# Kernel tuning notes

Hardware: AMD Instinct MI355X
Metric: run time of the kernel (lower is better)

The kernel has to match this reference:

```python
import jax, jax.numpy as jnp
import numpy as np

H = 128          # hidden
L = 4            # num PNA layers
NG = 32          # graphs in the batch
OUT = 12
N_NODES = 30000
N_EDGES = 480000
IN_NODE = 64
IN_EDGE = 16
EPS_BN = 1e-5
EPS_STD = 1e-5
# deg histogram torch.tensor([1,2,3,4,5,6]): cnt_i nodes have degree i
_cnt = np.arange(1.0, 7.0)
AVG_LOG = float((np.log(np.arange(6) + 1.0) * _cnt).sum() / _cnt.sum())


def _lin(k, fan_in, fan_out):
    return jax.random.normal(k, (fan_in, fan_out), jnp.float32) * 0.05


def setup_inputs() -> dict:
    key = jax.random.key(0)
    ks = jax.random.split(key, 16)
    d = {}
    d["x"] = jax.random.normal(ks[0], (N_NODES, IN_NODE), jnp.float32)
    d["edge_attr"] = jax.random.normal(ks[1], (N_EDGES, IN_EDGE), jnp.float32)
    d["edge_index"] = jax.random.randint(ks[2], (2, N_EDGES), 0, N_NODES)
    d["batch"] = jnp.sort(jax.random.randint(ks[3], (N_NODES,), 0, NG))
    d["node_emb_W"] = _lin(ks[4], IN_NODE, H)
    d["node_emb_b"] = jnp.zeros((H,), jnp.float32)
    d["edge_emb_W"] = _lin(ks[5], IN_EDGE, H)
    d["edge_emb_b"] = jnp.zeros((H,), jnp.float32)
    kl = jax.random.split(ks[6], 4 * L)
    d["edge_enc_W"] = jnp.stack([_lin(kl[i], H, H) for i in range(L)])
    d["edge_enc_b"] = jnp.zeros((L, H), jnp.float32)
    d["pre_W"] = jnp.stack([_lin(kl[L + i], 3 * H, H) for i in range(L)])
    d["pre_b"] = jnp.zeros((L, H), jnp.float32)
    d["post_W"] = jnp.stack([_lin(kl[2 * L + i], 13 * H, H) for i in range(L)])
    d["post_b"] = jnp.zeros((L, H), jnp.float32)
    d["lin_W"] = jnp.stack([_lin(kl[3 * L + i], H, H) for i in range(L)])
    d["lin_b"] = jnp.zeros((L, H), jnp.float32)
    d["bn_gamma"] = jnp.ones((L, H), jnp.float32)
    d["bn_beta"] = jnp.zeros((L, H), jnp.float32)
    d["head1_W"] = _lin(ks[7], H, H // 2)
    d["head1_b"] = jnp.zeros((H // 2,), jnp.float32)
    d["head2_W"] = _lin(ks[8], H // 2, OUT)
    d["head2_b"] = jnp.zeros((OUT,), jnp.float32)
    return d


def _pna_layer(x, e, src, dst, eW, eb, pW, pb, oW, ob, lW, lb):
    n = x.shape[0]
    ee = e @ eW + eb                                      # edge encoder [E, H]
    h = jnp.concatenate([x[dst], x[src], ee], axis=-1)    # (x_i, x_j, e) [E, 3H]
    m = h @ pW + pb                                       # pre-nn messages [E, H]
    ones = jnp.ones((m.shape[0],), m.dtype)
    deg = jax.ops.segment_sum(ones, dst, num_segments=n)  # in-degree [N]
    degc = jnp.maximum(deg, 1.0)[:, None]
    has = (deg > 0.0)[:, None]
    mean = jax.ops.segment_sum(m, dst, num_segments=n) / degc
    mn = jnp.where(has, jax.ops.segment_min(m, dst, num_segments=n), 0.0)
    mx = jnp.where(has, jax.ops.segment_max(m, dst, num_segments=n), 0.0)
    mean_sq = jax.ops.segment_sum(m * m, dst, num_segments=n) / degc
    std = jnp.sqrt(jax.nn.relu(mean_sq - mean * mean) + EPS_STD)
    agg = jnp.concatenate([mean, mn, mx, std], axis=-1)   # aggregators [N, 4H]
    amp = jnp.log(degc + 1.0) / AVG_LOG                   # amplification scale
    out = jnp.concatenate([agg, agg * amp, agg / amp], axis=-1)  # id/amp/atten [N, 12H]
    out = jnp.concatenate([x, out], axis=-1) @ oW + ob    # post-nn [N, H]
    return out @ lW + lb                                  # final lin


def reference(x, edge_index, batch, edge_attr, node_emb_W, node_emb_b,
              edge_emb_W, edge_emb_b, edge_enc_W, edge_enc_b, pre_W, pre_b,
              post_W, post_b, lin_W, lin_b, bn_gamma, bn_beta,
              head1_W, head1_b, head2_W, head2_b):
    src, dst = edge_index[0], edge_index[1]
    h = x @ node_emb_W + node_emb_b
    e = edge_attr @ edge_emb_W + edge_emb_b
    for l in range(L):
        h = _pna_layer(h, e, src, dst, edge_enc_W[l], edge_enc_b[l],
                       pre_W[l], pre_b[l], post_W[l], post_b[l],
                       lin_W[l], lin_b[l])
        mu = h.mean(axis=0)
        var = h.var(axis=0)  # biased, as BatchNorm training-mode normalization
        h = (h - mu) / jnp.sqrt(var + EPS_BN) * bn_gamma[l] + bn_beta[l]
        h = jax.nn.relu(h)   # dropout == identity (eval mode reference)
    g = jax.ops.segment_sum(h, batch, num_segments=NG)   # global_add_pool [NG, H]
    z = jax.nn.relu(g @ head1_W + head1_b)
    return z @ head2_W + head2_b
```

## Files before the change

kernel.cpp:

```cpp
#include <hip/hip_runtime.h>
#include <hip/hip_bf16.h>
#include <math.h>

#define NN 30000
#define NE 480000
#define NLAYER 4
#define NGR 32
#define NOUT 12
#define EPS_BN 1e-5f
#define EPS_STD 1e-5f
#define AVG_LOG 1.3821454785305053f
#define MB_GRID 235

typedef unsigned short ushort_t;
typedef __bf16 bf16x8 __attribute__((ext_vector_type(8)));
typedef float floatx4 __attribute__((ext_vector_type(4)));

__device__ __forceinline__ float bfu(ushort_t u){
  union { unsigned int ui; float f; } c; c.ui = ((unsigned int)u) << 16; return c.f;
}
__device__ __forceinline__ ushort_t f2bf(float f){
  union { float f; unsigned int u; } c; c.f = f;
  unsigned int lsb = (c.u >> 16) & 1u;
  c.u += 0x7FFFu + lsb;
  return (ushort_t)(c.u >> 16);
}

__device__ __forceinline__ int plausible(unsigned int bits32){
  unsigned int e = (bits32 >> 23) & 0xFF;
  if(e == 0xFF) return 0;
  if(bits32 == 0 || bits32 == 0x80000000u) return 1;
  return (e >= 93 && e <= 140) ? 1 : 0;
}

__global__ void k_detect(const ushort_t* __restrict__ xr, int* __restrict__ flag){
  __shared__ int cnt[2];
  if(threadIdx.x < 2) cnt[threadIdx.x] = 0;
  __syncthreads();
  const unsigned int* xf = (const unsigned int*)xr;
  int gf = 0, gb = 0;
  for(int i = threadIdx.x; i < 1024; i += 256){
    gf += plausible(xf[i]);
    gb += plausible(((unsigned int)xr[i]) << 16);
  }
  atomicAdd(&cnt[0], gf);
  atomicAdd(&cnt[1], gb);
  __syncthreads();
  if(threadIdx.x == 0) *flag = (cnt[1] >= cnt[0]) ? 1 : 0;
}

#define NJOBS 18
struct CvtJob { const void* s; float* d; int n; };
struct CvtArgs { CvtJob j[NJOBS]; const int* flag; };

__global__ void k_cvt(CvtArgs a){
  int ji = blockIdx.y;
  const int isbf = *a.flag;
  float* d = a.j[ji].d;
  int n = a.j[ji].n;
  if(isbf){
    const ushort_t* s = (const ushort_t*)a.j[ji].s;
    for(int i = blockIdx.x*256 + threadIdx.x; i < n; i += gridDim.x*256) d[i] = bfu(s[i]);
  } else {
    const float* s = (const float*)a.j[ji].s;
    for(int i = blockIdx.x*256 + threadIdx.x; i < n; i += gridDim.x*256) d[i] = s[i];
  }
}

__global__ void k_xbf(const void* __restrict__ x, ushort_t* __restrict__ d,
                      const int* __restrict__ flag){
  int i = blockIdx.x*256 + threadIdx.x;
  if(i >= NN*64) return;
  if(*flag) d[i] = ((const ushort_t*)x)[i];
  else      d[i] = f2bf(((const float*)x)[i]);
}

#define NTR 9
struct TrJob { const float* s; ushort_t* d; int K, N; };
struct TrArgs { TrJob j[NTR]; };

__global__ void k_tr(TrArgs a){
  TrJob j = a.j[blockIdx.y];
  int nk = j.K >> 6, nn = j.N >> 6;
  int tile = blockIdx.x;
  if(tile >= nk*nn) return;
  int tk = tile % nk, tn = tile / nk;
  int k0 = tk*64, n0 = tn*64;
  __shared__ float t[64][65];
  int w = threadIdx.x >> 6, c = threadIdx.x & 63;
  #pragma unroll
  for(int i=0;i<16;i+=1){
    int r = i*4 + w;
    t[r][c] = j.s[(size_t)(k0+r)*j.N + n0 + c];
  }
  __syncthreads();
  #pragma unroll
  for(int i=0;i<16;i+=1){
    int r = i*4 + w;
    j.d[(size_t)(n0+r)*j.K + k0 + c] = f2bf(t[c][r]);
  }
}

#define NFOLD 16
struct FoldJob { const float* s1; const float* s2; ushort_t* d; int Kd; };
struct FoldArgs { FoldJob j[NFOLD]; };

__global__ void k_fold(FoldArgs a){
  FoldJob j = a.j[blockIdx.y];
  const int n0 = blockIdx.x*16;
  __shared__ float s2s[128][16];
  int tid = threadIdx.x;
  for(int idx = tid; idx < 128*16; idx += 256){
    int t = idx >> 4, jj = idx & 15;
    s2s[t][jj] = j.s2[t*128 + n0 + jj];
  }
  __syncthreads();
  for(int k = tid; k < j.Kd; k += 256){
    float part[16];
    #pragma unroll
    for(int p=0;p<16;p++) part[p] = 0.f;
    for(int t0=0; t0<128; t0+=32){
      float rr[32];
      #pragma unroll
      for(int tt=0;tt<32;tt++) rr[tt] = j.s1[(size_t)k*128 + t0 + tt];
      #pragma unroll
      for(int p=0;p<16;p++){
        float acc = 0.f;
        #pragma unroll
        for(int tt=0;tt<32;tt++) acc += rr[tt]*s2s[t0+tt][p];
        part[p] += acc;
      }
    }
    #pragma unroll
    for(int p=0;p<16;p++)
      j.d[(size_t)(n0+p)*j.Kd + k] = f2bf(part[p]);
  }
}

__global__ void k_foldb(const float* __restrict__ postB, const float* __restrict__ linW,
                        const float* __restrict__ linB, float* __restrict__ biasY){
  int l = blockIdx.x, c = threadIdx.x;
  float a = linB[l*128+c];
  const float* L = linW + (size_t)l*128*128;
  const float* pb = postB + l*128;
  for(int t=0;t<128;t++) a += pb[t]*L[t*128+c];
  biasY[l*128+c] = a;
}

__global__ void k_deg(const int* __restrict__ dst, int* __restrict__ deg){
  int i = blockIdx.x*256 + threadIdx.x;
  if(i < NE){
    unsigned d = (unsigned)dst[i];
    if(d < NN) atomicAdd(&deg[d], 1);
  }
}

__global__ void k_scan1(const int* __restrict__ deg, int* __restrict__ rp,
                        int* __restrict__ bsum){
  __shared__ int wsum[16];
  int tid = threadIdx.x, lane = tid & 63, wid = tid >> 6;
  int i = blockIdx.x*1024 + tid;
  int v = (i < NN) ? deg[i] : 0;
  int incl = v;
  #pragma unroll
  for(int off=1; off<64; off<<=1){
    int t = __shfl_up(incl, off, 64);
    if(lane >= off) incl += t;
  }
  if(lane==63) wsum[wid] = incl;
  __syncthreads();
  int woff = 0;
  for(int w=0; w<wid; w++) woff += wsum[w];
  if(i < NN) rp[i+1] = incl + woff;
  if(tid == 0){
    int t = 0;
    for(int w=0; w<16; w++) t += wsum[w];
    bsum[blockIdx.x] = t;
  }
}

__global__ void k_scan2(const int* __restrict__ bsum, int* __restrict__ boff,
                        int* __restrict__ rp, int nb){
  if(threadIdx.x == 0){
    int run = 0;
    for(int b=0;b<nb;b++){ boff[b] = run; run += bsum[b]; }
    rp[0] = 0;
  }
}

__global__ void k_scan3(int* __restrict__ rp, const int* __restrict__ boff){
  int i = blockIdx.x*1024 + threadIdx.x;
  if(i < NN) rp[i+1] += boff[blockIdx.x];
}

__global__ void k_scatter(const int* __restrict__ dst,
                          const int* __restrict__ rp, int* __restrict__ fill,
                          int* __restrict__ eix_csr){
  int i = blockIdx.x*256 + threadIdx.x;
  if(i >= NE) return;
  unsigned d = (unsigned)dst[i];
  if(d >= NN) return;
  int pos = rp[d] + atomicAdd(&fill[d], 1);
  eix_csr[pos] = i;
}

__launch_bounds__(64)
__global__ void k_srt(const int* __restrict__ rp, int* __restrict__ eix){
  __shared__ int buf[64][129];
  int t = threadIdx.x;
  int n = blockIdx.x*64 + t;
  if(n >= NN) return;
  int s0 = rp[n], e0 = rp[n+1], d = e0 - s0;
  if(d <= 1) return;
  if(d <= 128){
    int* b = buf[t];
    for(int i=0;i<d;i++) b[i] = eix[s0+i];
    for(int i=1;i<d;i++){
      int k = b[i], j = i-1;
      while(j >= 0 && b[j] > k){ b[j+1] = b[j]; j--; }
      b[j+1] = k;
    }
    for(int i=0;i<d;i++) eix[s0+i] = b[i];
  } else {
    for(int i=s0+1;i<e0;i++){
      int k = eix[i], j = i-1;
      while(j >= s0 && eix[j] > k){ eix[j+1] = eix[j]; j--; }
      eix[j+1] = k;
    }
  }
}

__global__ void k_gather_ea(const int* __restrict__ eix, const int* __restrict__ esrc,
                            const void* __restrict__ ea,
                            ushort_t* __restrict__ out, int* __restrict__ src_csr,
                            const int* __restrict__ flag){
  int j = blockIdx.x*128 + threadIdx.x;
  if(j >= NE) return;
  int i = eix[j];
  src_csr[j] = esrc[i];
  uint4* d = (uint4*)(out + (size_t)j*16);
  if(*flag){
    const uint4* s = (const uint4*)((const ushort_t*)ea + (size_t)i*16);
    d[0] = s[0]; d[1] = s[1];
  } else {
    const float* s = (const float*)ea + (size_t)i*16;
    union { ushort_t us[16]; uint4 u4[2]; } pk;
    #pragma unroll
    for(int k=0;k<16;k++) pk.us[k] = f2bf(s[k]);
    d[0] = pk.u4[0]; d[1] = pk.u4[1];
  }
}

__global__ void k_prep_K(const float* __restrict__ embW, const float* __restrict__ embB,
                         const float* __restrict__ encW, const float* __restrict__ encB,
                         const float* __restrict__ preW, const float* __restrict__ preB,
                         float* __restrict__ Kf){
  int bx = blockIdx.x;
  int l = bx / 17, r = bx % 17;
  int c = threadIdx.x;
  const float* eW = encW + (size_t)l*128*128;
  const float* P3 = preW + (size_t)l*384*128 + 256*128;
  __shared__ float trow[128];
  float a;
  if(r < 16){
    a = 0.f;
    const float* w = embW + r*128;
    for(int k=0;k<128;k++) a += w[k]*eW[k*128+c];
  } else {
    a = encB[l*128+c];
    for(int k=0;k<128;k++) a += embB[k]*eW[k*128+c];
  }
  trow[c] = a;
  __syncthreads();
  float o = (r==16) ? preB[l*128+c] : 0.f;
  for(int k=0;k<128;k++) o += trow[k]*P3[k*128+c];
  Kf[(size_t)l*17*128 + r*128 + c] = o;
}

template<int EPI, int OUTBF>
__launch_bounds__(256)
__global__ void k_mm(const ushort_t* __restrict__ A, const ushort_t* __restrict__ BT,
                     void* __restrict__ C, void* __restrict__ C2,
                     int M, int K, int ldc, const float* __restrict__ bias){
  __shared__ __align__(16) ushort_t Als[128][88];
  __shared__ __align__(16) ushort_t Bls[128][88];
  const int tid = threadIdx.x;
  const int m0 = blockIdx.x*128, n0 = blockIdx.y*128;
  const int w = tid >> 6, lane = tid & 63;
  const int wm = (w & 1)*64, wn = (w >> 1)*64;
  const int quad = lane >> 4, l15 = lane & 15;
  floatx4 acc[4][4] = {};

  for(int k0=0; k0<K; k0+=64){
    #pragma unroll
    for(int i=0;i<4;i++){
      int c = tid + 256*i;
      int row = c >> 3, kc = (c & 7)*8;
      uint4 va = make_uint4(0u,0u,0u,0u);
      int gr = m0 + row;
      if(gr < M) va = *(const uint4*)(A + (size_t)gr*K + k0 + kc);
      *(uint4*)(&Als[row][kc]) = va;
      uint4 vb = *(const uint4*)(BT + (size_t)(n0+row)*K + k0 + kc);
      *(uint4*)(&Bls[row][kc]) = vb;
    }
    __syncthreads();
    #pragma unroll
    for(int ks=0; ks<64; ks+=32){
      bf16x8 a[4], b[4];
      #pragma unroll
      for(int i=0;i<4;i++) a[i] = *(const bf16x8*)(&Als[wm+16*i+l15][ks+quad*8]);
      #pragma unroll
      for(int j=0;j<4;j++) b[j] = *(const bf16x8*)(&Bls[wn+16*j+l15][ks+quad*8]);
      #pragma unroll
      for(int i=0;i<4;i++)
        #pragma unroll
        for(int j=0;j<4;j++)
          acc[i][j] = __builtin_amdgcn_mfma_f32_16x16x32_bf16(a[i], b[j], acc[i][j], 0, 0, 0);
    }
    __syncthreads();
  }

  #pragma unroll
  for(int i=0;i<4;i++){
    #pragma unroll
    for(int r=0;r<4;r++){
      int grow = m0 + wm + 16*i + quad*4 + r;
      if(grow >= M) continue;
      #pragma unroll
      for(int j=0;j<4;j++){
        int gcol = n0 + wn + 16*j + l15;
        float v = acc[i][j][r];
        if(EPI==0){
          if(bias) v += bias[gcol];
          if(OUTBF) ((ushort_t*)C)[(size_t)grow*ldc + gcol] = f2bf(v);
          else      ((float*)  C)[(size_t)grow*ldc + gcol] = v;
        } else {
          if(n0 == 0) ((float*)C)[(size_t)grow*128 + gcol] = v;
          else        ((ushort_t*)C2)[(size_t)grow*128 + (gcol-128)] = f2bf(v);
        }
      }
    }
  }
}

__launch_bounds__(256)
__global__ void k_post(const ushort_t* __restrict__ aggb, const ushort_t* __restrict__ h,
                       const ushort_t* __restrict__ Wcat, const ushort_t* __restrict__ W0,
                       const float* __restrict__ biasY,
                       const float* __restrict__ ampv, const float* __restrict__ invv,
                       ushort_t* __restrict__ y, float* __restrict__ bnpart){
  __shared__ __align__(16) ushort_t Als[128][88];
  __shared__ __align__(16) ushort_t Bls[128][88];
  __shared__ float s_part[8][128];
  __shared__ float q_part[8][128];
  __shared__ float amp_s[128];
  __shared__ float inv_s[128];
  const int tid = threadIdx.x;
  const int m0 = blockIdx.x*128;
  const int w = tid >> 6, lane = tid & 63;
  const int wm = (w & 1)*64, wn = (w >> 1)*64;
  const int quad = lane >> 4, l15 = lane & 15;
  if(tid < 128){
    int rr = min(m0 + tid, NN-1);
    amp_s[tid] = ampv[rr];
    inv_s[tid] = invv[rr];
  }
  floatx4 accY[4][4] = {};

  for(int p=0; p<3; p++){
    floatx4 accP[4][4] = {};
    floatx4 (*tgt)[4] = (p==0) ? accY : accP;
    const ushort_t* Wp = Wcat + (size_t)p*128*512;
    for(int k0=0; k0<512; k0+=64){
      #pragma unroll
      for(int i=0;i<4;i++){
        int c = tid + 256*i;
        int row = c >> 3, kc = (c & 7)*8;
        uint4 va = make_uint4(0u,0u,0u,0u);
        int gr = m0 + row;
        if(gr < NN) va = *(const uint4*)(aggb + (size_t)gr*512 + k0 + kc);
        *(uint4*)(&Als[row][kc]) = va;
        uint4 vb = *(const uint4*)(Wp + (size_t)row*512 + k0 + kc);
        *(uint4*)(&Bls[row][kc]) = vb;
      }
      __syncthreads();
      #pragma unroll
      for(int ks=0; ks<64; ks+=32){
        bf16x8 a[4], b[4];
        #pragma unroll
        for(int i=0;i<4;i++) a[i] = *(const bf16x8*)(&Als[wm+16*i+l15][ks+quad*8]);
        #pragma unroll
        for(int j=0;j<4;j++) b[j] = *(const bf16x8*)(&Bls[wn+16*j+l15][ks+quad*8]);
        #pragma unroll
        for(int i=0;i<4;i++)
          #pragma unroll
          for(int j=0;j<4;j++)
            tgt[i][j] = __builtin_amdgcn_mfma_f32_16x16x32_bf16(a[i], b[j], tgt[i][j], 0, 0, 0);
      }
      __syncthreads();
    }
    if(p > 0){
      const float* cs = (p==1) ? amp_s : inv_s;
      #pragma unroll
      for(int i=0;i<4;i++)
        #pragma unroll
        for(int r=0;r<4;r++){
          float coef = cs[wm + 16*i + quad*4 + r];
          #pragma unroll
          for(int j=0;j<4;j++) accY[i][j][r] += coef*accP[i][j][r];
        }
    }
  }

  for(int k0=0; k0<128; k0+=64){
    #pragma unroll
    for(int i=0;i<4;i++){
      int c = tid + 256*i;
      int row = c >> 3, kc = (c & 7)*8;
      uint4 va = make_uint4(0u,0u,0u,0u);
      int gr = m0 + row;
      if(gr < NN) va = *(const uint4*)(h + (size_t)gr*128 + k0 + kc);
      *(uint4*)(&Als[row][kc]) = va;
      uint4 vb = *(const uint4*)(W0 + (size_t)row*128 + k0 + kc);
      *(uint4*)(&Bls[row][kc]) = vb;
    }
    __syncthreads();
    #pragma unroll
    for(int ks=0; ks<64; ks+=32){
      bf16x8 a[4], b[4];
      #pragma unroll
      for(int i=0;i<4;i++) a[i] = *(const bf16x8*)(&Als[wm+16*i+l15][ks+quad*8]);
      #pragma unroll
      for(int j=0;j<4;j++) b[j] = *(const bf16x8*)(&Bls[wn+16*j+l15][ks+quad*8]);
      #pragma unroll
      for(int i=0;i<4;i++)
        #pragma unroll
        for(int j=0;j<4;j++)
          accY[i][j] = __builtin_amdgcn_mfma_f32_16x16x32_bf16(a[i], b[j], accY[i][j], 0, 0, 0);
    }
    __syncthreads();
  }

  float s[4] = {0,0,0,0}, q[4] = {0,0,0,0};
  #pragma unroll
  for(int i=0;i<4;i++){
    #pragma unroll
    for(int r=0;r<4;r++){
      int grow = m0 + wm + 16*i + quad*4 + r;
      if(grow >= NN) continue;
      #pragma unroll
      for(int j=0;j<4;j++){
        int gcol = wn + 16*j + l15;
        float v = accY[i][j][r] + biasY[gcol];
        y[(size_t)grow*128 + gcol] = f2bf(v);
        s[j] += v; q[j] += v*v;
      }
    }
  }
  const int slot = (w & 1)*4 + quad;
  #pragma unroll
  for(int j=0;j<4;j++){
    s_part[slot][wn + 16*j + l15] = s[j];
    q_part[slot][wn + 16*j + l15] = q[j];
  }
  __syncthreads();
  if(tid < 128){
    float ss = 0.f, qq = 0.f;
    #pragma unroll
    for(int sl=0; sl<8; sl++){ ss += s_part[sl][tid]; qq += q_part[sl][tid]; }
    bnpart[(size_t)blockIdx.x*256 + tid]       = ss;
    bnpart[(size_t)blockIdx.x*256 + 128 + tid] = qq;
  }
}

__launch_bounds__(128)
__global__ void k_agg(const int* __restrict__ rp, const int* __restrict__ src_csr,
                      const ushort_t* __restrict__ ea_csr, const float* __restrict__ Kf,
                      const float* __restrict__ Ah, const ushort_t* __restrict__ Bh,
                      ushort_t* __restrict__ agg, float* __restrict__ ampv,
                      float* __restrict__ invv){
  const int n = blockIdx.x, c = threadIdx.x;
  const int s0 = rp[n], e0 = rp[n+1];
  const int deg = e0 - s0;
  float kcol[16];
  #pragma unroll
  for(int k=0;k<16;k++) kcol[k] = Kf[k*128+c];
  const float base = Ah[(size_t)n*128 + c] + Kf[16*128+c];
  float sum=0.f, sq=0.f, mn=INFINITY, mx=-INFINITY;
  __shared__ float ea_s[16][16];
  __shared__ int src_s[16];
  for(int j0=s0; j0<e0; j0+=16){
    int cnt = min(16, e0-j0);
    __syncthreads();
    int ee = c>>4, kk = c&15;
    if(ee < cnt)   ea_s[ee][kk]   = bfu(ea_csr[(size_t)(j0+ee)*16+kk]);
    if(ee+8 < cnt) ea_s[ee+8][kk] = bfu(ea_csr[(size_t)(j0+ee+8)*16+kk]);
    if(c < cnt) src_s[c] = src_csr[j0+c];
    __syncthreads();
    for(int e=0;e<cnt;e++){
      float m = base + bfu(Bh[(size_t)src_s[e]*128 + c]);
      #pragma unroll
      for(int k=0;k<16;k++) m += ea_s[e][k]*kcol[k];
      sum += m; sq += m*m; mn = fminf(mn,m); mx = fmaxf(mx,m);
    }
  }
  float degc = (float)(deg>0?deg:1);
  float mean = sum/degc;
  float var  = fmaxf(sq/degc - mean*mean, 0.f);
  float sd = sqrtf(var + EPS_STD);
  if(deg==0){ mn=0.f; mx=0.f; }
  ushort_t* o = agg + (size_t)n*512;
  o[c]     = f2bf(mean);
  o[128+c] = f2bf(mn);
  o[256+c] = f2bf(mx);
  o[384+c] = f2bf(sd);
  if(c==0){
    float amp = logf(degc+1.f)/AVG_LOG;
    ampv[n] = amp; invv[n] = 1.f/amp;
  }
}

__global__ void k_bn_fin(const float* __restrict__ bnpart, int nb,
                         const float* __restrict__ gamma, const float* __restrict__ beta,
                         float* __restrict__ scale, float* __restrict__ shift){
  int c = threadIdx.x;
  float s0=0.f,s1=0.f,s2=0.f,s3=0.f, q0=0.f,q1=0.f,q2=0.f,q3=0.f;
  int b = 0;
  for(; b+3<nb; b+=4){
    s0 += bnpart[(size_t)(b+0)*256 + c];       q0 += bnpart[(size_t)(b+0)*256 + 128 + c];
    s1 += bnpart[(size_t)(b+1)*256 + c];       q1 += bnpart[(size_t)(b+1)*256 + 128 + c];
    s2 += bnpart[(size_t)(b+2)*256 + c];       q2 += bnpart[(size_t)(b+2)*256 + 128 + c];
    s3 += bnpart[(size_t)(b+3)*256 + c];       q3 += bnpart[(size_t)(b+3)*256 + 128 + c];
  }
  for(; b<nb; b++){ s0 += bnpart[(size_t)b*256 + c]; q0 += bnpart[(size_t)b*256 + 128 + c]; }
  float s = (s0+s1)+(s2+s3), q = (q0+q1)+(q2+q3);
  float mu  = s*(1.f/NN);
  float var = fmaxf(q*(1.f/NN) - mu*mu, 0.f);
  float inv = 1.f/sqrtf(var + EPS_BN);
  float sc = gamma[c]*inv;
  scale[c] = sc;
  shift[c] = beta[c] - mu*sc;
}

__global__ void k_bn_relu(const ushort_t* __restrict__ y, const float* __restrict__ scale,
                          const float* __restrict__ shift, ushort_t* __restrict__ h){
  int i = blockIdx.x*256 + threadIdx.x;
  if(i >= NN*128) return;
  int c = i & 127;
  float v = fmaxf(bfu(y[i])*scale[c] + shift[c], 0.f);
  h[i] = f2bf(v);
}

__device__ __forceinline__ int lbound(const int* a, int n, int v){
  int lo = 0, hi = n;
  while(lo < hi){ int mid = (lo+hi) >> 1; if(a[mid] < v) lo = mid+1; else hi = mid; }
  return lo;
}

__launch_bounds__(128)
__global__ void k_pool1(const ushort_t* __restrict__ h, const int* __restrict__ batch,
                        float* __restrict__ gpart){
  int b = blockIdx.x, ch = blockIdx.y, c = threadIdx.x;
  int lo = lbound(batch, NN, b), hi = lbound(batch, NN, b+1);
  int len = hi - lo;
  int per = (len + 7) >> 3;
  int r0 = min(lo + ch*per, hi);
  int r1 = min(r0 + per, hi);
  float acc = 0.f;
  for(int r=r0;r<r1;r++) acc += bfu(h[(size_t)r*128+c]);
  gpart[((size_t)b*8 + ch)*128 + c] = acc;
}

__global__ void k_pool2(const float* __restrict__ gpart, float* __restrict__ g){
  int b = blockIdx.x, c = threadIdx.x;
  float acc = 0.f;
  #pragma unroll
  for(int ch=0; ch<8; ch++) acc += gpart[((size_t)b*8 + ch)*128 + c];
  g[(size_t)b*128 + c] = acc;
}

__launch_bounds__(64)
__global__ void k_head(const float* __restrict__ g, const float* __restrict__ W1,
                       const float* __restrict__ b1, const float* __restrict__ W2,
                       const float* __restrict__ b2, void* __restrict__ out,
                       const int* __restrict__ flag){
  __shared__ float gs[128];
  __shared__ float zs[64];
  int r = blockIdx.x, tid = threadIdx.x;
  gs[tid] = g[r*128 + tid];
  gs[tid+64] = g[r*128 + tid + 64];
  __syncthreads();
  float a = b1[tid];
  for(int k=0;k<128;k++) a += gs[k]*W1[k*64+tid];
  zs[tid] = fmaxf(a, 0.f);
  __syncthreads();
  if(tid < NOUT){
    float o = b2[tid];
    for(int k=0;k<64;k++) o += zs[k]*W2[k*12+tid];
    if(*flag) ((ushort_t*)out)[r*NOUT + tid] = f2bf(o);
    else      ((float*)out)[r*NOUT + tid] = o;
  }
}

extern "C" void kernel_launch(void* const* d_in, const int* in_sizes, int n_in,
                              void* d_out, int out_size, void* d_ws, size_t ws_size,
                              hipStream_t stream){
  const void* x_raw = d_in[0];
  const void* ea_raw;
  const int*  eidx;
  const int*  batch;
  if(in_sizes[1] == 2*NE){
    eidx   = (const int*)d_in[1];
    batch  = (const int*)d_in[2];
    ea_raw = d_in[3];
  } else {
    ea_raw = d_in[1];
    eidx   = (const int*)d_in[2];
    batch  = (const int*)d_in[3];
  }
  const void* nembW_r = d_in[4];
  const void* nembB_r = d_in[5];
  const void* eembW_r = d_in[6];
  const void* eembB_r = d_in[7];
  const void* encW_r  = d_in[8];
  const void* encB_r  = d_in[9];
  const void* preW_r  = d_in[10];
  const void* preB_r  = d_in[11];
  const void* postW_r = d_in[12];
  const void* postB_r = d_in[13];
  const void* linW_r  = d_in[14];
  const void* linB_r  = d_in[15];
  const void* bnG_r   = d_in[16];
  const void* bnB_r   = d_in[17];
  const void* h1W_r   = d_in[18];
  const void* h1B_r   = d_in[19];
  const void* h2W_r   = d_in[20];
  const void* h2B_r   = d_in[21];

  char* p = (char*)d_ws;
  auto alloc = [&](size_t bytes)->void*{
    void* r = (void*)p; p += (bytes + 255) & ~(size_t)255; return r;
  };
  int*      dtflag  = (int*)     alloc(sizeof(int)*16);
  int*      deg     = (int*)     alloc(sizeof(int)*NN);
  int*      fill    = (int*)     alloc(sizeof(int)*NN);
  int*      rp      = (int*)     alloc(sizeof(int)*(NN+1));
  int*      bsum    = (int*)     alloc(sizeof(int)*64);
  int*      boff    = (int*)     alloc(sizeof(int)*64);
  int*      src_csr = (int*)     alloc(sizeof(int)*NE);
  int*      eix_csr = (int*)     alloc(sizeof(int)*NE);
  ushort_t* ea_csr  = (ushort_t*)alloc(sizeof(ushort_t)*(size_t)NE*16);
  ushort_t* xbf     = (ushort_t*)alloc(sizeof(ushort_t)*(size_t)NN*64);
  ushort_t* h       = (ushort_t*)alloc(sizeof(ushort_t)*(size_t)NN*128);
  ushort_t* aggb    = (ushort_t*)alloc(sizeof(ushort_t)*(size_t)NN*512);
  float*    Ah      = (float*)   alloc(sizeof(float)*(size_t)NN*128);
  ushort_t* Bh      = (ushort_t*)alloc(sizeof(ushort_t)*(size_t)NN*128);
  ushort_t* y       = (ushort_t*)alloc(sizeof(ushort_t)*(size_t)NN*128);
  float*    ampv    = (float*)   alloc(sizeof(float)*(NN+256));
  float*    invv    = (float*)   alloc(sizeof(float)*(NN+256));
  float*    Kf      = (float*)   alloc(sizeof(float)*4*17*128);
  float*    bnpart  = (float*)   alloc(sizeof(float)*(size_t)MB_GRID*256);
  float*    bnscale = (float*)   alloc(sizeof(float)*128);
  float*    bnshift = (float*)   alloc(sizeof(float)*128);
  float*    gpart   = (float*)   alloc(sizeof(float)*32*8*128);
  float*    g       = (float*)   alloc(sizeof(float)*32*128);
  float*    biasY   = (float*)   alloc(sizeof(float)*4*128);
  ushort_t* WembT   = (ushort_t*)alloc(sizeof(ushort_t)*128*64);
  ushort_t* P12T    = (ushort_t*)alloc(sizeof(ushort_t)*4*256*128);
  ushort_t* WcatFT  = (ushort_t*)alloc(sizeof(ushort_t)*(size_t)4*384*512);
  ushort_t* W0FT    = (ushort_t*)alloc(sizeof(ushort_t)*4*128*128);
  float* nembW = (float*)alloc(sizeof(float)*64*128);
  float* nembB = (float*)alloc(sizeof(float)*128);
  float* eembW = (float*)alloc(sizeof(float)*16*128);
  float* eembB = (float*)alloc(sizeof(float)*128);
  float* encW  = (float*)alloc(sizeof(float)*4*128*128);
  float* encB  = (float*)alloc(sizeof(float)*4*128);
  float* preW  = (float*)alloc(sizeof(float)*4*384*128);
  float* preB  = (float*)alloc(sizeof(float)*4*128);
  float* postW = (float*)alloc(sizeof(float)*(size_t)4*1664*128);
  float* postB = (float*)alloc(sizeof(float)*4*128);
  float* linW  = (float*)alloc(sizeof(float)*4*128*128);
  float* linB  = (float*)alloc(sizeof(float)*4*128);
  float* bnG   = (float*)alloc(sizeof(float)*4*128);
  float* bnB   = (float*)alloc(sizeof(float)*4*128);
  float* h1W   = (float*)alloc(sizeof(float)*128*64);
  float* h1B   = (float*)alloc(sizeof(float)*64);
  float* h2W   = (float*)alloc(sizeof(float)*64*12);
  float* h2B   = (float*)alloc(sizeof(float)*12);

  CvtArgs ca;
  ca.flag = dtflag;
  int ji = 0;
  auto job = [&](const void* s, float* d, int n){ ca.j[ji].s=s; ca.j[ji].d=d; ca.j[ji].n=n; ji++; };
  job(nembW_r, nembW, 64*128);
  job(nembB_r, nembB, 128);
  job(eembW_r, eembW, 16*128);
  job(eembB_r, eembB, 128);
  job(encW_r,  encW,  4*128*128);
  job(encB_r,  encB,  4*128);
  job(preW_r,  preW,  4*384*128);
  job(preB_r,  preB,  4*128);
  job(postW_r, postW, 4*1664*128);
  job(postB_r, postB, 4*128);
  job(linW_r,  linW,  4*128*128);
  job(linB_r,  linB,  4*128);
  job(bnG_r,   bnG,   4*128);
  job(bnB_r,   bnB,   4*128);
  job(h1W_r,   h1W,   128*64);
  job(h1B_r,   h1B,   64);
  job(h2W_r,   h2W,   64*12);
  job(h2B_r,   h2B,   12);

  TrArgs ta;
  int ti = 0;
  auto tj = [&](const float* s, ushort_t* d, int K, int N){ ta.j[ti].s=s; ta.j[ti].d=d; ta.j[ti].K=K; ta.j[ti].N=N; ti++; };
  tj(nembW, WembT, 64, 128);
  for(int l=0;l<4;l++){
    const float* pw = preW + (size_t)l*384*128;
    tj(pw,           P12T + (size_t)l*256*128,           128, 128);
    tj(pw + 128*128, P12T + (size_t)l*256*128 + 128*128, 128, 128);
  }

  FoldArgs fa;
  int fi = 0;
  for(int l=0;l<4;l++){
    const float* po = postW + (size_t)l*1664*128;
    const float* L  = linW + (size_t)l*128*128;
    for(int b=0;b<3;b++){
      fa.j[fi].s1 = po + (size_t)(128 + b*512)*128;
      fa.j[fi].s2 = L;
      fa.j[fi].d  = WcatFT + (size_t)l*384*512 + (size_t)b*128*512;
      fa.j[fi].Kd = 512;
      fi++;
    }
    fa.j[fi].s1 = po;
    fa.j[fi].s2 = L;
    fa.j[fi].d  = W0FT + (size_t)l*128*128;
    fa.j[fi].Kd = 128;
    fi++;
  }

  const int* esrc = eidx;
  const int* edst = eidx + NE;

  hipMemsetAsync(deg, 0, sizeof(int)*NN, stream);
  hipMemsetAsync(fill, 0, sizeof(int)*NN, stream);

  k_detect<<<1, 256, 0, stream>>>((const ushort_t*)x_raw, dtflag);
  k_cvt<<<dim3(128, NJOBS), 256, 0, stream>>>(ca);
  k_xbf<<<(NN*64+255)/256, 256, 0, stream>>>(x_raw, xbf, dtflag);
  k_tr<<<dim3(4, NTR), 256, 0, stream>>>(ta);
  k_fold<<<dim3(8, NFOLD), 256, 0, stream>>>(fa);
  k_foldb<<<4, 128, 0, stream>>>(postB, linW, linB, biasY);
  k_prep_K<<<68, 128, 0, stream>>>(eembW, eembB, encW, encB, preW, preB, Kf);

  k_deg<<<(NE+255)/256, 256, 0, stream>>>(edst, deg);
  k_scan1<<<30, 1024, 0, stream>>>(deg, rp, bsum);
  k_scan2<<<1, 64, 0, stream>>>(bsum, boff, rp, 30);
  k_scan3<<<30, 1024, 0, stream>>>(rp, boff);
  k_scatter<<<(NE+255)/256, 256, 0, stream>>>(edst, rp, fill, eix_csr);
  k_srt<<<(NN+63)/64, 64, 0, stream>>>(rp, eix_csr);
  k_gather_ea<<<(NE+127)/128, 128, 0, stream>>>(eix_csr, esrc, ea_raw, ea_csr, src_csr, dtflag);

  k_mm<0,1><<<dim3(MB_GRID,1), 256, 0, stream>>>(xbf, WembT, h, nullptr, NN, 64, 128, nembB);

  for(int l=0; l<NLAYER; l++){
    k_mm<2,0><<<dim3(MB_GRID,2), 256, 0, stream>>>(h, P12T + (size_t)l*256*128, Ah, Bh,
                                                   NN, 128, 128, nullptr);
    k_agg<<<NN, 128, 0, stream>>>(rp, src_csr, ea_csr, Kf + (size_t)l*17*128,
                                  Ah, Bh, aggb, ampv, invv);
    k_post<<<MB_GRID, 256, 0, stream>>>(aggb, h, WcatFT + (size_t)l*384*512,
                                        W0FT + (size_t)l*128*128, biasY + l*128,
                                        ampv, invv, y, bnpart);
    k_bn_fin<<<1, 128, 0, stream>>>(bnpart, MB_GRID, bnG + l*128, bnB + l*128,
                                    bnscale, bnshift);
    k_bn_relu<<<(NN*128+255)/256, 256, 0, stream>>>(y, bnscale, bnshift, h);
  }

  k_pool1<<<dim3(NGR,8), 128, 0, stream>>>(h, batch, gpart);
  k_pool2<<<NGR, 128, 0, stream>>>(gpart, g);
  k_head<<<NGR, 64, 0, stream>>>(g, h1W, h1B, h2W, h2B, d_out, dtflag);
}
```

Before: 1.031 ms.

## Use MFMA for per-edge encoder projection in aggregation; halve post GEMM row tile

The aggregation kernel now computes the 16-wide edge-attribute projection for a batch of 16 edges with one bf16 MFMA per 16-column tile, using weight fragments pre-packed by a new prep kernel. Before, each thread did 16 scalar FMAs per edge. Per-lane min/max/sum partials are then combined across quads with shuffles. Separately, the post-NN GEMM tile drops from 128 to 64 rows, doubling its grid to 469 blocks for better CU coverage, at the cost of reloading the weight tile twice as often. The edge projection now rounds weights to bf16, which slightly lowers precision, and Bh is loaded even for padded edges.

```diff
diff --git a/kernel.cpp b/kernel.cpp
--- a/kernel.cpp
+++ b/kernel.cpp
@@ -11,6 +11,7 @@
 #define EPS_STD 1e-5f
 #define AVG_LOG 1.3821454785305053f
 #define MB_GRID 235
+#define MB2 469
 
 typedef unsigned short ushort_t;
 typedef __bf16 bf16x8 __attribute__((ext_vector_type(8)));
@@ -277,6 +278,26 @@
   Kf[(size_t)l*17*128 + r*128 + c] = o;
 }
 
+__global__ void k_prep_Kfrag(const float* __restrict__ Kf, ushort_t* __restrict__ KfT,
+                             float* __restrict__ Kfb){
+  int b = blockIdx.x;
+  int l = b >> 3, t = b & 7;
+  int lane = threadIdx.x;
+  int quad = lane >> 4, l15 = lane & 15;
+  const float* K = Kf + (size_t)l*17*128;
+  ushort_t* o = KfT + (((size_t)l*8 + t)*64 + lane)*8;
+  #pragma unroll
+  for(int j=0;j<8;j++){
+    int k = quad*8 + j;
+    int col = t*16 + l15;
+    o[j] = (k < 16) ? f2bf(K[k*128 + col]) : (ushort_t)0;
+  }
+  if(t == 0){
+    Kfb[l*128 + lane]      = K[16*128 + lane];
+    Kfb[l*128 + lane + 64] = K[16*128 + lane + 64];
+  }
+}
+
 template<int EPI, int OUTBF>
 __launch_bounds__(256)
 __global__ void k_mm(const ushort_t* __restrict__ A, const ushort_t* __restrict__ BT,
@@ -349,52 +370,56 @@
                        const float* __restrict__ biasY,
                        const float* __restrict__ ampv, const float* __restrict__ invv,
                        ushort_t* __restrict__ y, float* __restrict__ bnpart){
-  __shared__ __align__(16) ushort_t Als[128][88];
+  __shared__ __align__(16) ushort_t Als[64][88];
   __shared__ __align__(16) ushort_t Bls[128][88];
-  __shared__ float s_part[8][128];
-  __shared__ float q_part[8][128];
-  __shared__ float amp_s[128];
-  __shared__ float inv_s[128];
+  __shared__ float s_part[4][128];
+  __shared__ float q_part[4][128];
+  __shared__ float amp_s[64];
+  __shared__ float inv_s[64];
   const int tid = threadIdx.x;
-  const int m0 = blockIdx.x*128;
+  const int m0 = blockIdx.x*64;
   const int w = tid >> 6, lane = tid & 63;
-  const int wm = (w & 1)*64, wn = (w >> 1)*64;
   const int quad = lane >> 4, l15 = lane & 15;
-  if(tid < 128){
+  const int cw = w*32;
+  if(tid < 64){
     int rr = min(m0 + tid, NN-1);
     amp_s[tid] = ampv[rr];
     inv_s[tid] = invv[rr];
   }
-  floatx4 accY[4][4] = {};
+  floatx4 accY[4][2] = {};
 
   for(int p=0; p<3; p++){
-    floatx4 accP[4][4] = {};
-    floatx4 (*tgt)[4] = (p==0) ? accY : accP;
+    floatx4 accP[4][2] = {};
+    floatx4 (*tgt)[2] = (p==0) ? accY : accP;
     const ushort_t* Wp = Wcat + (size_t)p*128*512;
     for(int k0=0; k0<512; k0+=64){
       #pragma unroll
-      for(int i=0;i<4;i++){
+      for(int i=0;i<2;i++){
         int c = tid + 256*i;
         int row = c >> 3, kc = (c & 7)*8;
         uint4 va = make_uint4(0u,0u,0u,0u);
         int gr = m0 + row;
         if(gr < NN) va = *(const uint4*)(aggb + (size_t)gr*512 + k0 + kc);
         *(uint4*)(&Als[row][kc]) = va;
-        uint4 vb = *(const uint4*)(Wp + (size_t)row*512 + k0 + kc);
-        *(uint4*)(&Bls[row][kc]) = vb;
+      }
+      #pragma unroll
+      for(int i=0;i<4;i++){
+        int c = tid + 256*i;
+        int row = c >> 3, kc = (c & 7)*8;
+        *(uint4*)(&Bls[row][kc]) = *(const uint4*)(Wp + (size_t)row*512 + k0 + kc);
       }
       __syncthreads();
       #pragma unroll
       for(int ks=0; ks<64; ks+=32){
-        bf16x8 a[4], b[4];
+        bf16x8 a[4], b[2];
         #pragma unroll
-        for(int i=0;i<4;i++) a[i] = *(const bf16x8*)(&Als[wm+16*i+l15][ks+quad*8]);
+        for(int i=0;i<4;i++) a[i] = *(const bf16x8*)(&Als[16*i+l15][ks+quad*8]);
         #pragma unroll
-        for(int j=0;j<4;j++) b[j] = *(const bf16x8*)(&Bls[wn+16*j+l15][ks+quad*8]);
+        for(int j=0;j<2;j++) b[j] = *(const bf16x8*)(&Bls[cw+16*j+l15][ks+quad*8]);
         #pragma unroll
         for(int i=0;i<4;i++)
           #pragma unroll
-          for(int j=0;j<4;j++)
+          for(int j=0;j<2;j++)
             tgt[i][j] = __builtin_amdgcn_mfma_f32_16x16x32_bf16(a[i], b[j], tgt[i][j], 0, 0, 0);
       }
       __syncthreads();
@@ -405,69 +430,72 @@
       for(int i=0;i<4;i++)
         #pragma unroll
         for(int r=0;r<4;r++){
-          float coef = cs[wm + 16*i + quad*4 + r];
+          float coef = cs[16*i + quad*4 + r];
           #pragma unroll
-          for(int j=0;j<4;j++) accY[i][j][r] += coef*accP[i][j][r];
+          for(int j=0;j<2;j++) accY[i][j][r] += coef*accP[i][j][r];
         }
     }
   }
 
   for(int k0=0; k0<128; k0+=64){
     #pragma unroll
-    for(int i=0;i<4;i++){
+    for(int i=0;i<2;i++){
       int c = tid + 256*i;
       int row = c >> 3, kc = (c & 7)*8;
       uint4 va = make_uint4(0u,0u,0u,0u);
       int gr = m0 + row;
       if(gr < NN) va = *(const uint4*)(h + (size_t)gr*128 + k0 + kc);
       *(uint4*)(&Als[row][kc]) = va;
-      uint4 vb = *(const uint4*)(W0 + (size_t)row*128 + k0 + kc);
-      *(uint4*)(&Bls[row][kc]) = vb;
+    }
+    #pragma unroll
+    for(int i=0;i<4;i++){
+      int c = tid + 256*i;
+      int row = c >> 3, kc = (c & 7)*8;
+      *(uint4*)(&Bls[row][kc]) = *(const uint4*)(W0 + (size_t)row*128 + k0 + kc);
     }
     __syncthreads();
     #pragma unroll
     for(int ks=0; ks<64; ks+=32){
-      bf16x8 a[4], b[4];
-      #pragma unroll
-      for(int i=0;i<4;i++) a[i] = *(const bf16x8*)(&Als[wm+16*i+l15][ks+quad*8]);
-      #pragma unroll
-      for(int j=0;j<4;j++) b[j] = *(const bf16x8*)(&Bls[wn+16*j+l15][ks+quad*8]);
+      bf16x8 a[4], b[2];
+      #pragma unroll
+      for(int i=0;i<4;i++) a[i] = *(const bf16x8*)(&Als[16*i+l15][ks+quad*8]);
+      #pragma unroll
+      for(int j=0;j<2;j++) b[j] = *(const bf16x8*)(&Bls[cw+16*j+l15][ks+quad*8]);
       #pragma unroll
       for(int i=0;i<4;i++)
         #pragma unroll
-        for(int j=0;j<4;j++)
+        for(int j=0;j<2;j++)
           accY[i][j] = __builtin_amdgcn_mfma_f32_16x16x32_bf16(a[i], b[j], accY[i][j], 0, 0, 0);
     }
     __syncthreads();
   }
 
-  float s[4] = {0,0,0,0}, q[4] = {0,0,0,0};
+  float s[2] = {0,0}, q[2] = {0,0};
   #pragma unroll
   for(int i=0;i<4;i++){
     #pragma unroll
     for(int r=0;r<4;r++){
-      int grow = m0 + wm + 16*i + quad*4 + r;
+      int grow = m0 + 16*i + quad*4 + r;
       if(grow >= NN) continue;
       #pragma unroll
-      for(int j=0;j<4;j++){
-        int gcol = wn + 16*j + l15;
+      for(int j=0;j<2;j++){
+        int gcol = cw + 16*j + l15;
         float v = accY[i][j][r] + biasY[gcol];
         y[(size_t)grow*128 + gcol] = f2bf(v);
         s[j] += v; q[j] += v*v;
       }
     }
   }
-  const int slot = (w & 1)*4 + quad;
-  #pragma unroll
-  for(int j=0;j<4;j++){
-    s_part[slot][wn + 16*j + l15] = s[j];
-    q_part[slot][wn + 16*j + l15] = q[j];
+  #pragma unroll
+  for(int j=0;j<2;j++){
+    s_part[quad][cw + 16*j + l15] = s[j];
+    q_part[quad][cw + 16*j + l15] = q[j];
   }
   __syncthreads();
   if(tid < 128){
     float ss = 0.f, qq = 0.f;
     #pragma unroll
-    for(int sl=0; sl<8; sl++){ ss += s_part[sl][tid]; qq += q_part[sl][tid]; }
+    for(int sl=0; sl<4; sl++){ ss += s_part[sl][tid]; qq += q_part[sl][tid]; }
     bnpart[(size_t)blockIdx.x*256 + tid]       = ss;
     bnpart[(size_t)blockIdx.x*256 + 128 + tid] = qq;
   }
@@ -475,46 +503,86 @@
 
 __launch_bounds__(128)
 __global__ void k_agg(const int* __restrict__ rp, const int* __restrict__ src_csr,
-                      const ushort_t* __restrict__ ea_csr, const float* __restrict__ Kf,
+                      const ushort_t* __restrict__ ea_csr,
+                      const ushort_t* __restrict__ KfT, const float* __restrict__ Kfb,
                       const float* __restrict__ Ah, const ushort_t* __restrict__ Bh,
                       ushort_t* __restrict__ agg, float* __restrict__ ampv,
                       float* __restrict__ invv){
-  const int n = blockIdx.x, c = threadIdx.x;
-  const int s0 = rp[n], e0 = rp[n+1];
-  const int deg = e0 - s0;
-  float kcol[16];
-  #pragma unroll
-  for(int k=0;k<16;k++) kcol[k] = Kf[k*128+c];
-  const float base = Ah[(size_t)n*128 + c] + Kf[16*128+c];
-  float sum=0.f, sq=0.f, mn=INFINITY, mx=-INFINITY;
-  __shared__ float ea_s[16][16];
+  const int n = blockIdx.x, tid = threadIdx.x;
+  const int wv = tid >> 6, lane = tid & 63;
+  const int quad = lane >> 4, l15 = lane & 15;
+  const int s0 = rp[n], e0 = rp[n+1], deg = e0 - s0;
+  bf16x8 kf[4];
+  float base[4];
+  #pragma unroll
+  for(int tt=0;tt<4;tt++){
+    int t = wv*4 + tt;
+    kf[tt] = *(const bf16x8*)(KfT + ((size_t)t*64 + lane)*8);
+    int col = wv*64 + tt*16 + l15;
+    base[tt] = Ah[(size_t)n*128 + col] + Kfb[col];
+  }
+  float sum[4], sq[4], mn[4], mx[4];
+  #pragma unroll
+  for(int tt=0;tt<4;tt++){ sum[tt]=0.f; sq[tt]=0.f; mn[tt]=INFINITY; mx[tt]=-INFINITY; }
+  __shared__ __align__(16) ushort_t ea_s[16][16];
   __shared__ int src_s[16];
+
   for(int j0=s0; j0<e0; j0+=16){
     int cnt = min(16, e0-j0);
     __syncthreads();
-    int ee = c>>4, kk = c&15;
-    if(ee < cnt)   ea_s[ee][kk]   = bfu(ea_csr[(size_t)(j0+ee)*16+kk]);
-    if(ee+8 < cnt) ea_s[ee+8][kk] = bfu(ea_csr[(size_t)(j0+ee+8)*16+kk]);
-    if(c < cnt) src_s[c] = src_csr[j0+c];
+    {
+      int edge = tid >> 3, pos = (tid & 7)*2;
+      int se = j0 + min(edge, cnt-1);
+      *(unsigned int*)(&ea_s[edge][pos]) = *(const unsigned int*)(ea_csr + (size_t)se*16 + pos);
+    }
+    if(tid < 16) src_s[tid] = src_csr[min(j0+tid, e0-1)];
     __syncthreads();
-    for(int e=0;e<cnt;e++){
-      float m = base + bfu(Bh[(size_t)src_s[e]*128 + c]);
-      #pragma unroll
-      for(int k=0;k<16;k++) m += ea_s[e][k]*kcol[k];
-      sum += m; sq += m*m; mn = fminf(mn,m); mx = fmaxf(mx,m);
-    }
-  }
-  float degc = (float)(deg>0?deg:1);
-  float mean = sum/degc;
-  float var  = fmaxf(sq/degc - mean*mean, 0.f);
-  float sd = sqrtf(var + EPS_STD);
-  if(deg==0){ mn=0.f; mx=0.f; }
-  ushort_t* o = agg + (size_t)n*512;
-  o[c]     = f2bf(mean);
-  o[128+c] = f2bf(mn);
-  o[256+c] = f2bf(mx);
-  o[384+c] = f2bf(sd);
-  if(c==0){
+    bf16x8 af = {};
+    if(quad < 2) af = *(const bf16x8*)(&ea_s[l15][quad*8]);
+    #pragma unroll
+    for(int tt=0;tt<4;tt++){
+      floatx4 zc = {0.f,0.f,0.f,0.f};
+      floatx4 em = __builtin_amdgcn_mfma_f32_16x16x32_bf16(af, kf[tt], zc, 0, 0, 0);
+      int col = wv*64 + tt*16 + l15;
+      #pragma unroll
+      for(int r=0;r<4;r++){
+        int e = quad*4 + r;
+        float bh = bfu(Bh[(size_t)src_s[e]*128 + col]);
+        float m = base[tt] + bh + em[r];
+        if(e < cnt){
+          sum[tt] += m; sq[tt] += m*m;
+          mn[tt] = fminf(mn[tt], m); mx[tt] = fmaxf(mx[tt], m);
+        }
+      }
+    }
+  }
+
+  #pragma unroll
+  for(int tt=0;tt<4;tt++){
+    sum[tt] += __shfl_xor(sum[tt], 16); sum[tt] += __shfl_xor(sum[tt], 32);
+    sq[tt]  += __shfl_xor(sq[tt], 16);  sq[tt]  += __shfl_xor(sq[tt], 32);
+    mn[tt] = fminf(mn[tt], __shfl_xor(mn[tt], 16)); mn[tt] = fminf(mn[tt], __shfl_xor(mn[tt], 32));
+    mx[tt] = fmaxf(mx[tt], __shfl_xor(mx[tt], 16)); mx[tt] = fmaxf(mx[tt], __shfl_xor(mx[tt], 32));
+  }
+  if(quad == 0){
+    float degc = (float)(deg>0?deg:1);
+    ushort_t* o = agg + (size_t)n*512;
+    #pragma unroll
+    for(int tt=0;tt<4;tt++){
+      int col = wv*64 + tt*16 + l15;
+      float mean = sum[tt]/degc;
+      float var = fmaxf(sq[tt]/degc - mean*mean, 0.f);
+      float sd = sqrtf(var + EPS_STD);
+      float lmn = (deg==0) ? 0.f : mn[tt];
+      float lmx = (deg==0) ? 0.f : mx[tt];
+      o[col]       = f2bf(mean);
+      o[128 + col] = f2bf(lmn);
+      o[256 + col] = f2bf(lmx);
+      o[384 + col] = f2bf(sd);
+    }
+  }
+  if(tid == 0){
+    float degc = (float)(deg>0?deg:1);
     float amp = logf(degc+1.f)/AVG_LOG;
     ampv[n] = amp; invv[n] = 1.f/amp;
   }
@@ -659,7 +727,9 @@
   float*    ampv    = (float*)   alloc(sizeof(float)*(NN+256));
   float*    invv    = (float*)   alloc(sizeof(float)*(NN+256));
   float*    Kf      = (float*)   alloc(sizeof(float)*4*17*128);
-  float*    bnpart  = (float*)   alloc(sizeof(float)*(size_t)MB_GRID*256);
+  ushort_t* KfTf    = (ushort_t*)alloc(sizeof(ushort_t)*4*8*64*8);
+  float*    Kfb     = (float*)   alloc(sizeof(float)*4*128);
+  float*    bnpart  = (float*)   alloc(sizeof(float)*(size_t)MB2*256);
   float*    bnscale = (float*)   alloc(sizeof(float)*128);
   float*    bnshift = (float*)   alloc(sizeof(float)*128);
   float*    gpart   = (float*)   alloc(sizeof(float)*32*8*128);
@@ -753,6 +823,7 @@
   k_fold<<<dim3(8, NFOLD), 256, 0, stream>>>(fa);
   k_foldb<<<4, 128, 0, stream>>>(postB, linW, linB, biasY);
   k_prep_K<<<68, 128, 0, stream>>>(eembW, eembB, encW, encB, preW, preB, Kf);
+  k_prep_Kfrag<<<32, 64, 0, stream>>>(Kf, KfTf, Kfb);
 
   k_deg<<<(NE+255)/256, 256, 0, stream>>>(edst, deg);
   k_scan1<<<30, 1024, 0, stream>>>(deg, rp, bsum);
@@ -767,12 +838,13 @@
   for(int l=0; l<NLAYER; l++){
     k_mm<2,0><<<dim3(MB_GRID,2), 256, 0, stream>>>(h, P12T + (size_t)l*256*128, Ah, Bh,
                                                    NN, 128, 128, nullptr);
-    k_agg<<<NN, 128, 0, stream>>>(rp, src_csr, ea_csr, Kf + (size_t)l*17*128,
+    k_agg<<<NN, 128, 0, stream>>>(rp, src_csr, ea_csr,
+                                  KfTf + (size_t)l*8*64*8, Kfb + l*128,
                                   Ah, Bh, aggb, ampv, invv);
-    k_post<<<MB_GRID, 256, 0, stream>>>(aggb, h, WcatFT + (size_t)l*384*512,
-                                        W0FT + (size_t)l*128*128, biasY + l*128,
-                                        ampv, invv, y, bnpart);
-    k_bn_fin<<<1, 128, 0, stream>>>(bnpart, MB_GRID, bnG + l*128, bnB + l*128,
+    k_post<<<MB2, 256, 0, stream>>>(aggb, h, WcatFT + (size_t)l*384*512,
+                                    W0FT + (size_t)l*128*128, biasY + l*128,
+                                    ampv, invv, y, bnpart);
+    k_bn_fin<<<1, 128, 0, stream>>>(bnpart, MB2, bnG + l*128, bnB + l*128,
                                     bnscale, bnshift);
     k_bn_relu<<<(NN*128+255)/256, 256, 0, stream>>>(y, bnscale, bnshift, h);
   }
```

Result: slower. 1.054 ms (+2.2%).
